# Kernel tuning notes

Hardware: AMD Instinct MI355X
Metric: run time of the kernel (lower is better)

Reference implementation:

```python
import jax, jax.numpy as jnp
import numpy as np

N = 10000       # nodes
F_IN = 512      # input_features
E_DIM = 256     # embedding_features
H0, H1 = 512, 256  # fc layer widths (layers=[512,256]); fc input = 2*E_DIM = 512
N_EDGES = 160000


def setup_inputs() -> dict:
    key = jax.random.key(0)
    ks = jax.random.split(key, 10)
    feature = jax.random.normal(ks[0], (N, F_IN), jnp.float32)
    edge_src = jax.random.randint(ks[1], (N_EDGES,), 0, N, jnp.int32)
    edge_dst = jax.random.randint(ks[2], (N_EDGES,), 0, N, jnp.int32)
    def lin(k, fan_in, fan_out):
        return jax.random.normal(k, (fan_in, fan_out), jnp.float32) / np.sqrt(fan_in).astype(np.float32)
    We = lin(ks[3], F_IN, E_DIM);     be = jnp.zeros((E_DIM,), jnp.float32)
    W0 = lin(ks[4], 2 * E_DIM, H0);   b0 = jnp.zeros((H0,), jnp.float32)
    W1 = lin(ks[5], H0, H1);          b1 = jnp.zeros((H1,), jnp.float32)
    Wlk = lin(ks[6], H1, 1);          blk = jnp.zeros((1,), jnp.float32)
    Wa = lin(ks[7], H1, 2);           ba = jnp.zeros((2,), jnp.float32)
    return dict(feature=feature, We=We, be=be, W0=W0, b0=b0, W1=W1, b1=b1,
                Wlk=Wlk, blk=blk, Wa=Wa, ba=ba,
                edge_src=edge_src, edge_dst=edge_dst)


def reference(feature, We, be, W0, b0, W1, b1, Wlk, blk, Wa, ba, edge_src, edge_dst):
    # get_embedding: Linear + relu
    emb = jax.nn.relu(feature @ We + be)                      # [N, E]
    # Each node i has its neighbor entries plus one 'ending' entry paired with zeros
    seg = jnp.concatenate([edge_src, jnp.arange(N, dtype=edge_src.dtype)])     # [T]
    dst_all = jnp.concatenate([edge_dst, jnp.full((N,), -1, edge_dst.dtype)])  # -1 = ending sentinel
    nbr = jnp.concatenate([emb[edge_dst], jnp.zeros((N, E_DIM), emb.dtype)], axis=0)
    s = jnp.concatenate([emb[seg], nbr], axis=-1)             # [T, 2E]
    # fc MLP, then lk head
    h = jax.nn.relu(jax.nn.relu(s @ W0 + b0) @ W1 + b1)       # [T, H1]
    lk = (h @ Wlk + blk)[:, 0]                                # [T]
    # Deterministic greedy pick per node (argmax of lk == argmax of softmax(lk))
    best = jax.ops.segment_max(lk, seg, num_segments=N)       # [N]
    T = lk.shape[0]
    cand = jnp.where(lk == best[seg], jnp.arange(T, dtype=jnp.int32), -1)
    win = jax.ops.segment_max(cand, seg, num_segments=N)      # winning entry index per node
    chosen = dst_all[win]                                     # chosen neighbor (-1 = ending)
    # action head on the winning pair feature; argmax(softmax(logits)) == argmax(logits)
    logits = h[win] @ Wa + ba                                 # [N, 2]
    at = jnp.argmax(logits, axis=-1)
    do_upd = (chosen >= 0) & (at == 1)
    safe = jnp.clip(chosen, 0, N - 1)
    # hv = mean(feature_origin[i], feature_origin[chosen]) then re-embed
    mean_feat = 0.5 * (feature + feature[safe])               # [N, F]
    new_val = jax.nn.relu(mean_feat @ We + be)                # [N, E]
    tgt = jnp.where(do_upd, safe, N)                          # N = out of range -> dropped
    return emb.at[tgt].set(new_val, mode='drop')
```

## Files before the change

kernel.cpp:

```cpp
#include <hip/hip_runtime.h>
#include <stdint.h>

#define N_NODES 10000
#define F_IN    512
#define E_DIM   256
#define H0D     512
#define H1D     256
#define N_EDGES 160000
#define T_TOT   (N_EDGES + N_NODES)

#define MARGIN_LK 4e-3f
#define MARGIN_L  4e-3f
#define LIST_CAP 60000
#define FIX_GRID 512
#define LP 40

typedef _Float16 f16;
typedef __attribute__((ext_vector_type(8))) _Float16 f16x8;
typedef __attribute__((ext_vector_type(4))) _Float16 f16x4;
typedef __attribute__((ext_vector_type(4))) float f32x4;

__device__ __forceinline__ unsigned int f2ord(float f) {
    unsigned int u = __float_as_uint(f);
    return (u & 0x80000000u) ? ~u : (u | 0x80000000u);
}
__device__ __forceinline__ float ord2f(unsigned int o) {
    unsigned int u = (o & 0x80000000u) ? (o & 0x7fffffffu) : ~o;
    return __uint_as_float(u);
}

__global__ void k_prep_all(const float* __restrict__ We,
                           const float* __restrict__ W1,
                           const float* __restrict__ W0,
                           f16* __restrict__ WeC_h, f16* __restrict__ WeC_l,
                           f16* __restrict__ W1C_h, f16* __restrict__ W1C_l,
                           f16* __restrict__ W0C_h, f16* __restrict__ W0C_l) {
    int b = blockIdx.x;
    int n = threadIdx.x;
    const float* W;
    int ld, rowoff, colbase, c;
    f16 *dh_base, *dl_base;
    if (b < 16) {
        W = We; ld = E_DIM; rowoff = 0; colbase = 0; c = b;
        dh_base = WeC_h; dl_base = WeC_l;
    } else if (b < 32) {
        W = W1; ld = H1D; rowoff = 0; colbase = 0; c = b - 16;
        dh_base = W1C_h; dl_base = W1C_l;
    } else {
        int g = (b - 32) >> 3; c = (b - 32) & 7;
        rowoff = (g >= 2) ? 256 : 0; colbase = (g & 1) * 256;
        W = W0; ld = H0D;
        dh_base = W0C_h + (size_t)g * 8 * 256 * 32;
        dl_base = W0C_l + (size_t)g * 8 * 256 * 32;
    }
    f16* dh = dh_base + ((size_t)c * 256 + n) * 32;
    f16* dl = dl_base + ((size_t)c * 256 + n) * 32;
    const float* src = W + (size_t)(rowoff + c * 32) * ld + colbase + n;
#pragma unroll
    for (int kk = 0; kk < 32; kk++) {
        float w = src[(size_t)kk * ld];
        f16 h = (f16)w;
        f16 l = (f16)(w - (float)h);
        dh[kk] = h;
        dl[kk] = l;
    }
}

__global__ __launch_bounds__(256, 2) void k1_split(
        const float* __restrict__ feat, const f16* __restrict__ Bh_g,
        const f16* __restrict__ Bl_g, const float* __restrict__ be,
        float* __restrict__ Z, float* __restrict__ out) {
    __shared__ f16 Ah[32 * LP], Al_[32 * LP];
    const int tid = threadIdx.x;
    const int wave = tid >> 6, lane = tid & 63;
    const int quad = lane >> 4, l15 = lane & 15;
    const int mbase = blockIdx.x * 32;
    const int arow = tid >> 3, apos = tid & 7;
    const int gm_a = mbase + arow;
    const float* Arow = feat + (size_t)gm_a * F_IN + apos * 4;
    const bool rowok = (gm_a < N_NODES);

    f32x4 acc[2][4];
#pragma unroll
    for (int i = 0; i < 2; i++)
#pragma unroll
        for (int j = 0; j < 4; j++) acc[i][j] = (f32x4){0.f, 0.f, 0.f, 0.f};

    f16x8 bh[4], bl[4], bhn[4], bln[4];
#pragma unroll
    for (int ct = 0; ct < 4; ct++) {
        size_t o = ((size_t)(wave * 64 + ct * 16 + l15)) * 32 + quad * 8;
        bh[ct] = *(const f16x8*)(Bh_g + o);
        bl[ct] = *(const f16x8*)(Bl_g + o);
    }
    float4 a = rowok ? *(const float4*)(Arow) : make_float4(0.f, 0.f, 0.f, 0.f);

    for (int c = 0; c < 16; c++) {
        f16x4 hv, lv;
        float av[4] = {a.x, a.y, a.z, a.w};
#pragma unroll
        for (int q = 0; q < 4; q++) {
            f16 h = (f16)av[q];
            hv[q] = h;
            lv[q] = (f16)(av[q] - (float)h);
        }
        *(f16x4*)(Ah + arow * LP + apos * 4) = hv;
        *(f16x4*)(Al_ + arow * LP + apos * 4) = lv;
        if (c + 1 < 16) {
            a = rowok ? *(const float4*)(Arow + (c + 1) * 32)
                      : make_float4(0.f, 0.f, 0.f, 0.f);
#pragma unroll
            for (int ct = 0; ct < 4; ct++) {
                size_t o = ((size_t)((c + 1) * 256 + wave * 64 + ct * 16 + l15)) * 32 + quad * 8;
                bhn[ct] = *(const f16x8*)(Bh_g + o);
                bln[ct] = *(const f16x8*)(Bl_g + o);
            }
        }
        __syncthreads();
        f16x8 afh[2], afl[2];
#pragma unroll
        for (int rt = 0; rt < 2; rt++) {
            afh[rt] = *(const f16x8*)(Ah + (rt * 16 + l15) * LP + quad * 8);
            afl[rt] = *(const f16x8*)(Al_ + (rt * 16 + l15) * LP + quad * 8);
        }
#pragma unroll
        for (int rt = 0; rt < 2; rt++)
#pragma unroll
            for (int ct = 0; ct < 4; ct++) {
                acc[rt][ct] = __builtin_amdgcn_mfma_f32_16x16x32_f16(
                    afh[rt], bh[ct], acc[rt][ct], 0, 0, 0);
                acc[rt][ct] = __builtin_amdgcn_mfma_f32_16x16x32_f16(
                    afl[rt], bh[ct], acc[rt][ct], 0, 0, 0);
                acc[rt][ct] = __builtin_amdgcn_mfma_f32_16x16x32_f16(
                    afh[rt], bl[ct], acc[rt][ct], 0, 0, 0);
            }
        __syncthreads();
#pragma unroll
        for (int ct = 0; ct < 4; ct++) { bh[ct] = bhn[ct]; bl[ct] = bln[ct]; }
    }

#pragma unroll
    for (int ct = 0; ct < 4; ct++) {
        int n = wave * 64 + ct * 16 + l15;
        float bb = be[n];
#pragma unroll
        for (int rt = 0; rt < 2; rt++)
#pragma unroll
            for (int reg = 0; reg < 4; reg++) {
                int gm = mbase + rt * 16 + quad * 4 + reg;
                if (gm < N_NODES) {
                    float z = acc[rt][ct][reg] + bb;
                    Z[(size_t)gm * E_DIM + n] = z;
                    out[(size_t)gm * E_DIM + n] = fmaxf(z, 0.f);
                }
            }
    }
}

__global__ __launch_bounds__(256, 3) void k2_split(
        const float* __restrict__ emb, const f16* __restrict__ W0Ch,
        const f16* __restrict__ W0Cl, const float* __restrict__ b0,
        f16* __restrict__ Ph, f16* __restrict__ Pl,
        f16* __restrict__ Qh, f16* __restrict__ Ql) {
    __shared__ f16 Ah[64 * LP], Al_[64 * LP];
    const int tid = threadIdx.x;
    const int wave = tid >> 6, lane = tid & 63;
    const int quad = lane >> 4, l15 = lane & 15;
    const int mbase = blockIdx.x * 64;
    const int g = blockIdx.y;
    const int isQ = (g >= 2);
    const int colbase = (g & 1) * 256;
    const int arow = tid >> 2, akp = tid & 3;
    const int gm_a = mbase + arow;
    const float* Arow = emb + (size_t)gm_a * E_DIM + akp * 8;
    const bool rowok = (gm_a < N_NODES);
    const f16* Bh_g = W0Ch + (size_t)g * 8 * 256 * 32;
    const f16* Bl_g = W0Cl + (size_t)g * 8 * 256 * 32;

    f32x4 acc[4][4];
#pragma unroll
    for (int i = 0; i < 4; i++)
#pragma unroll
        for (int j = 0; j < 4; j++) acc[i][j] = (f32x4){0.f, 0.f, 0.f, 0.f};

    f16x8 bh[4], bl[4], bhn[4], bln[4];
#pragma unroll
    for (int ct = 0; ct < 4; ct++) {
        size_t o = ((size_t)(wave * 64 + ct * 16 + l15)) * 32 + quad * 8;
        bh[ct] = *(const f16x8*)(Bh_g + o);
        bl[ct] = *(const f16x8*)(Bl_g + o);
    }
    float4 a0 = make_float4(0.f, 0.f, 0.f, 0.f), a1 = a0;
    if (rowok) { a0 = *(const float4*)(Arow); a1 = *(const float4*)(Arow + 4); }

    for (int c = 0; c < 8; c++) {
        f16x8 hv, lv;
        float av[8] = {a0.x, a0.y, a0.z, a0.w, a1.x, a1.y, a1.z, a1.w};
#pragma unroll
        for (int q = 0; q < 8; q++) {
            f16 h = (f16)av[q];
            hv[q] = h;
            lv[q] = (f16)(av[q] - (float)h);
        }
        *(f16x8*)(Ah + arow * LP + akp * 8) = hv;
        *(f16x8*)(Al_ + arow * LP + akp * 8) = lv;
        if (c + 1 < 8) {
            if (rowok) {
                a0 = *(const float4*)(Arow + (c + 1) * 32);
                a1 = *(const float4*)(Arow + (c + 1) * 32 + 4);
            }
#pragma unroll
            for (int ct = 0; ct < 4; ct++) {
                size_t o = ((size_t)((c + 1) * 256 + wave * 64 + ct * 16 + l15)) * 32 + quad * 8;
                bhn[ct] = *(const f16x8*)(Bh_g + o);
                bln[ct] = *(const f16x8*)(Bl_g + o);
            }
        }
        __syncthreads();
        f16x8 afh[4], afl[4];
#pragma unroll
        for (int rt = 0; rt < 4; rt++) {
            afh[rt] = *(const f16x8*)(Ah + (rt * 16 + l15) * LP + quad * 8);
            afl[rt] = *(const f16x8*)(Al_ + (rt * 16 + l15) * LP + quad * 8);
        }
#pragma unroll
        for (int rt = 0; rt < 4; rt++)
#pragma unroll
            for (int ct = 0; ct < 4; ct++) {
                acc[rt][ct] = __builtin_amdgcn_mfma_f32_16x16x32_f16(
                    afh[rt], bh[ct], acc[rt][ct], 0, 0, 0);
                acc[rt][ct] = __builtin_amdgcn_mfma_f32_16x16x32_f16(
                    afl[rt], bh[ct], acc[rt][ct], 0, 0, 0);
                acc[rt][ct] = __builtin_amdgcn_mfma_f32_16x16x32_f16(
                    afh[rt], bl[ct], acc[rt][ct], 0, 0, 0);
            }
        __syncthreads();
#pragma unroll
        for (int ct = 0; ct < 4; ct++) { bh[ct] = bhn[ct]; bl[ct] = bln[ct]; }
    }

    f16* dh = isQ ? Qh : Ph;
    f16* dl = isQ ? Ql : Pl;
#pragma unroll
    for (int ct = 0; ct < 4; ct++) {
        int n = wave * 64 + ct * 16 + l15;
        float bb = isQ ? 0.f : b0[colbase + n];
#pragma unroll
        for (int rt = 0; rt < 4; rt++)
#pragma unroll
            for (int reg = 0; reg < 4; reg++) {
                int gm = mbase + rt * 16 + quad * 4 + reg;
                if (gm < N_NODES) {
                    float v = acc[rt][ct][reg] + bb;
                    f16 h = (f16)v;
                    dh[(size_t)gm * H0D + colbase + n] = h;
                    dl[(size_t)gm * H0D + colbase + n] = (f16)(v - (float)h);
                }
            }
    }
}

__global__ __launch_bounds__(256, 3) void k3_f16(
        const f16* __restrict__ Pf, const f16* __restrict__ Qf,
        const f16* __restrict__ W1Bh, const float* __restrict__ b1,
        const float* __restrict__ Wlk, const float* __restrict__ blkp,
        const float* __restrict__ Wa, const float* __restrict__ ba,
        const int* __restrict__ esrc, const int* __restrict__ edst,
        unsigned long long* __restrict__ keys, float* __restrict__ lk_app,
        float* __restrict__ logits) {
    __shared__ f16 Ah[64 * LP];
    __shared__ float redA[64][5], redB[64][5], redC[64][5];
    __shared__ int s_seg[64], s_dst[64];
    const int tid = threadIdx.x;
    const int wave = tid >> 6, lane = tid & 63;
    const int quad = lane >> 4, l15 = lane & 15;
    const int tbase = blockIdx.x * 64;

    if (tid < 64) {
        int t = tbase + tid;
        int s = 0, d = -1;
        if (t < N_EDGES) { s = esrc[t]; d = edst[t]; }
        else if (t < T_TOT) { s = t - N_EDGES; }
        s_seg[tid] = s;
        s_dst[tid] = d;
    }
    __syncthreads();

    const int arow = tid >> 2, akp = tid & 3;
    const int sA = s_seg[arow], dA = s_dst[arow];
    const f16* Prow = Pf + (size_t)sA * H0D + akp * 8;
    const f16* Qrow = Qf + (size_t)(dA >= 0 ? dA : 0) * H0D + akp * 8;
    const bool hasQ = (dA >= 0);
    const f16x8 zero8 = (f16x8)(f16)0;

    f32x4 acc[4][4];
#pragma unroll
    for (int i = 0; i < 4; i++)
#pragma unroll
        for (int j = 0; j < 4; j++) acc[i][j] = (f32x4){0.f, 0.f, 0.f, 0.f};

    f16x8 pa = *(const f16x8*)(Prow);
    f16x8 qa = hasQ ? *(const f16x8*)(Qrow) : zero8;
    f16x8 bf[4], bfn[4];
#pragma unroll
    for (int ct = 0; ct < 4; ct++)
        bf[ct] = *(const f16x8*)(W1Bh + ((size_t)(wave * 64 + ct * 16 + l15)) * 32 + quad * 8);

    for (int c = 0; c < 16; c++) {
        f16x8 hv;
#pragma unroll
        for (int q = 0; q < 8; q++) {
            f16 s = pa[q] + qa[q];
            hv[q] = (s > (f16)0) ? s : (f16)0;
        }
        *(f16x8*)(Ah + arow * LP + akp * 8) = hv;
        if (c + 1 < 16) {
            pa = *(const f16x8*)(Prow + (c + 1) * 32);
            qa = hasQ ? *(const f16x8*)(Qrow + (c + 1) * 32) : zero8;
#pragma unroll
            for (int ct = 0; ct < 4; ct++)
                bfn[ct] = *(const f16x8*)(W1Bh +
                    ((size_t)((c + 1) * 256 + wave * 64 + ct * 16 + l15)) * 32 + quad * 8);
        }
        __syncthreads();
        f16x8 af[4];
#pragma unroll
        for (int rt = 0; rt < 4; rt++)
            af[rt] = *(const f16x8*)(Ah + (rt * 16 + l15) * LP + quad * 8);
#pragma unroll
        for (int rt = 0; rt < 4; rt++)
#pragma unroll
            for (int ct = 0; ct < 4; ct++)
                acc[rt][ct] = __builtin_amdgcn_mfma_f32_16x16x32_f16(
                    af[rt], bf[ct], acc[rt][ct], 0, 0, 0);
        __syncthreads();
#pragma unroll
        for (int ct = 0; ct < 4; ct++) bf[ct] = bfn[ct];
    }

    float wl[4], wa0[4], wa1[4], bb[4];
#pragma unroll
    for (int ct = 0; ct < 4; ct++) {
        int n = wave * 64 + ct * 16 + l15;
        wl[ct] = Wlk[n];
        wa0[ct] = Wa[2 * n];
        wa1[ct] = Wa[2 * n + 1];
        bb[ct] = b1[n];
    }
#pragma unroll
    for (int rt = 0; rt < 4; rt++) {
#pragma unroll
        for (int reg = 0; reg < 4; reg++) {
            float plk = 0.f, p0 = 0.f, p1 = 0.f;
#pragma unroll
            for (int ct = 0; ct < 4; ct++) {
                float h = fmaxf(acc[rt][ct][reg] + bb[ct], 0.f);
                plk = fmaf(h, wl[ct], plk);
                p0 = fmaf(h, wa0[ct], p0);
                p1 = fmaf(h, wa1[ct], p1);
            }
#pragma unroll
            for (int off = 8; off >= 1; off >>= 1) {
                plk += __shfl_xor(plk, off);
                p0 += __shfl_xor(p0, off);
                p1 += __shfl_xor(p1, off);
            }
            if (l15 == 0) {
                int row = rt * 16 + quad * 4 + reg;
                redA[row][wave] = plk;
                redB[row][wave] = p0;
                redC[row][wave] = p1;
            }
        }
    }
    __syncthreads();
    if (tid < 64) {
        int t = tbase + tid;
        if (t < T_TOT) {
            float lk = redA[tid][0] + redA[tid][1] + redA[tid][2] + redA[tid][3] + blkp[0];
            float l0 = redB[tid][0] + redB[tid][1] + redB[tid][2] + redB[tid][3] + ba[0];
            float l1 = redC[tid][0] + redC[tid][1] + redC[tid][2] + redC[tid][3] + ba[1];
            lk_app[t] = lk;
            logits[2 * t] = l0;
            logits[2 * t + 1] = l1;
            unsigned long long key =
                ((unsigned long long)f2ord(lk) << 32) | (unsigned int)t;
            atomicMax(keys + s_seg[tid], key);
        }
    }
}

__global__ void k_gb(const float* __restrict__ lk_app,
                     const unsigned long long* __restrict__ keys,
                     const int* __restrict__ esrc,
                     const float* __restrict__ logits,
                     int* __restrict__ list, int* __restrict__ count) {
    int t = blockIdx.x * 256 + threadIdx.x;
    if (t < T_TOT) {
        int seg = (t < N_EDGES) ? esrc[t] : t - N_EDGES;
        unsigned long long k = keys[seg];
        int tw = (int)(k & 0xFFFFFFFFull);
        if (t != tw) {
            float best = ord2f((unsigned int)(k >> 32));
            if (lk_app[t] >= best - MARGIN_LK) {
                int idx = atomicAdd(count, 2);
                if (idx + 1 < LIST_CAP) { list[idx] = t; list[idx + 1] = tw; }
            }
        }
    }
    if (t < N_NODES) {
        int tw = (int)(keys[t] & 0xFFFFFFFFull);
        float g = fabsf(logits[2 * tw + 1] - logits[2 * tw]);
        if (g < MARGIN_L) {
            int idx = atomicAdd(count, 1);
            if (idx < LIST_CAP) list[idx] = tw;
        }
    }
}

__global__ __launch_bounds__(256, 2) void k_fix2(
        const f16* __restrict__ Ph, const f16* __restrict__ Pl,
        const f16* __restrict__ Qh, const f16* __restrict__ Ql,
        const f16* __restrict__ W1Ch, const f16* __restrict__ W1Cl,
        const float* __restrict__ b1, const float* __restrict__ Wlk,
        const float* __restrict__ blkp, const float* __restrict__ Wa,
        const float* __restrict__ ba, const int* __restrict__ esrc,
        const int* __restrict__ edst, const int* __restrict__ list,
        const int* __restrict__ count, unsigned long long* __restrict__ keys2,
        float* __restrict__ logits) {
    __shared__ f16 Ah[64 * LP], Al_[64 * LP];
    __shared__ float redA[64][5], redB[64][5], redC[64][5];
    __shared__ int s_seg[64], s_dst[64], s_t[64];
    const int tid = threadIdx.x;
    const int wave = tid >> 6, lane = tid & 63;
    const int quad = lane >> 4, l15 = lane & 15;
    int cnt = *count;
    if (cnt > LIST_CAP) cnt = LIST_CAP;
    const int nch = (cnt + 63) / 64;

    for (int ch = blockIdx.x; ch < nch; ch += gridDim.x) {
        if (tid < 64) {
            int li = ch * 64 + tid;
            int t = (li < cnt) ? list[li] : -1;
            int s = 0, d = -1;
            if (t >= 0 && t < T_TOT) {
                if (t < N_EDGES) { s = esrc[t]; d = edst[t]; }
                else { s = t - N_EDGES; }
            } else t = -1;
            s_t[tid] = t;
            s_seg[tid] = s;
            s_dst[tid] = d;
        }
        __syncthreads();

        const int arow = tid >> 2, akp = tid & 3;
        const int sA = s_seg[arow], dA = s_dst[arow];
        const f16* ph = Ph + (size_t)sA * H0D + akp * 8;
        const f16* pl = Pl + (size_t)sA * H0D + akp * 8;
        const f16* qh = Qh + (size_t)(dA >= 0 ? dA : 0) * H0D + akp * 8;
        const f16* ql = Ql + (size_t)(dA >= 0 ? dA : 0) * H0D + akp * 8;
        const bool hasQ = (dA >= 0);

        f32x4 acc[4][4];
#pragma unroll
        for (int i = 0; i < 4; i++)
#pragma unroll
            for (int j = 0; j < 4; j++) acc[i][j] = (f32x4){0.f, 0.f, 0.f, 0.f};

        for (int c = 0; c < 16; c++) {
            f16x8 vh = *(const f16x8*)(ph + c * 32);
            f16x8 vl = *(const f16x8*)(pl + c * 32);
            f16x8 wh, wlq;
            if (hasQ) {
                wh = *(const f16x8*)(qh + c * 32);
                wlq = *(const f16x8*)(ql + c * 32);
            }
            f16x8 hv, lv;
#pragma unroll
            for (int q = 0; q < 8; q++) {
                float v = (float)vh[q] + (float)vl[q];
                if (hasQ) v += (float)wh[q] + (float)wlq[q];
                v = fmaxf(v, 0.f);
                f16 h = (f16)v;
                hv[q] = h;
                lv[q] = (f16)(v - (float)h);
            }
            *(f16x8*)(Ah + arow * LP + akp * 8) = hv;
            *(f16x8*)(Al_ + arow * LP + akp * 8) = lv;
            f16x8 bh[4], bl[4];
#pragma unroll
            for (int ct = 0; ct < 4; ct++) {
                size_t o = ((size_t)(c * 256 + wave * 64 + ct * 16 + l15)) * 32 + quad * 8;
                bh[ct] = *(const f16x8*)(W1Ch + o);
                bl[ct] = *(const f16x8*)(W1Cl + o);
            }
            __syncthreads();
            f16x8 afh[4], afl[4];
#pragma unroll
            for (int rt = 0; rt < 4; rt++) {
                afh[rt] = *(const f16x8*)(Ah + (rt * 16 + l15) * LP + quad * 8);
                afl[rt] = *(const f16x8*)(Al_ + (rt * 16 + l15) * LP + quad * 8);
            }
#pragma unroll
            for (int rt = 0; rt < 4; rt++)
#pragma unroll
                for (int ct = 0; ct < 4; ct++) {
                    acc[rt][ct] = __builtin_amdgcn_mfma_f32_16x16x32_f16(
                        afh[rt], bh[ct], acc[rt][ct], 0, 0, 0);
                    acc[rt][ct] = __builtin_amdgcn_mfma_f32_16x16x32_f16(
                        afl[rt], bh[ct], acc[rt][ct], 0, 0, 0);
                    acc[rt][ct] = __builtin_amdgcn_mfma_f32_16x16x32_f16(
                        afh[rt], bl[ct], acc[rt][ct], 0, 0, 0);
                }
            __syncthreads();
        }

        float wl[4], wa0[4], wa1[4], bb[4];
#pragma unroll
        for (int ct = 0; ct < 4; ct++) {
            int n = wave * 64 + ct * 16 + l15;
            wl[ct] = Wlk[n];
            wa0[ct] = Wa[2 * n];
            wa1[ct] = Wa[2 * n + 1];
            bb[ct] = b1[n];
        }
#pragma unroll
        for (int rt = 0; rt < 4; rt++) {
#pragma unroll
            for (int reg = 0; reg < 4; reg++) {
                float plk = 0.f, p0 = 0.f, p1 = 0.f;
#pragma unroll
                for (int ct = 0; ct < 4; ct++) {
                    float h = fmaxf(acc[rt][ct][reg] + bb[ct], 0.f);
                    plk = fmaf(h, wl[ct], plk);
                    p0 = fmaf(h, wa0[ct], p0);
                    p1 = fmaf(h, wa1[ct], p1);
                }
#pragma unroll
                for (int off = 8; off >= 1; off >>= 1) {
                    plk += __shfl_xor(plk, off);
                    p0 += __shfl_xor(p0, off);
                    p1 += __shfl_xor(p1, off);
                }
                if (l15 == 0) {
                    int row = rt * 16 + quad * 4 + reg;
                    redA[row][wave] = plk;
                    redB[row][wave] = p0;
                    redC[row][wave] = p1;
                }
            }
        }
        __syncthreads();
        if (tid < 64) {
            int t = s_t[tid];
            if (t >= 0) {
                float lk = redA[tid][0] + redA[tid][1] + redA[tid][2] + redA[tid][3] + blkp[0];
                float l0 = redB[tid][0] + redB[tid][1] + redB[tid][2] + redB[tid][3] + ba[0];
                float l1 = redC[tid][0] + redC[tid][1] + redC[tid][2] + redC[tid][3] + ba[1];
                logits[2 * t] = l0;
                logits[2 * t + 1] = l1;
                unsigned long long key =
                    ((unsigned long long)f2ord(lk) << 32) | (unsigned int)t;
                atomicMax(keys2 + s_seg[tid], key);
            }
        }
        __syncthreads();
    }
}

__global__ void k4_select(const unsigned long long* __restrict__ keys,
                          const unsigned long long* __restrict__ keys2,
                          const int* __restrict__ edst,
                          const float* __restrict__ logits,
                          int* __restrict__ chosen_arr,
                          int* __restrict__ tgt_writer) {
    int i = blockIdx.x * 256 + threadIdx.x;
    if (i >= N_NODES) return;
    unsigned long long key = keys[i];
    unsigned long long k2v = keys2[i];
    if (k2v != 0ull) key = k2v;
    int t = (int)(key & 0xFFFFFFFFull);
    int chosen = (t < N_EDGES) ? edst[t] : -1;
    float lg0 = logits[2 * t], lg1 = logits[2 * t + 1];
    int at1 = (lg1 > lg0) ? 1 : 0;
    int c = (chosen >= 0 && at1) ? chosen : -1;
    chosen_arr[i] = c;
    if (c >= 0) atomicMax(tgt_writer + c, i + 1);
}

__global__ void k5_update(const int* __restrict__ chosen_arr,
                          const int* __restrict__ tgt_writer,
                          const float* __restrict__ Z,
                          float* __restrict__ out) {
    int i = blockIdx.x;
    int c = chosen_arr[i];
    if (c < 0 || tgt_writer[c] != i + 1) return;
    int n = threadIdx.x;
    float z = 0.5f * (Z[(size_t)i * E_DIM + n] + Z[(size_t)c * E_DIM + n]);
    out[(size_t)c * E_DIM + n] = fmaxf(z, 0.f);
}

extern "C" void kernel_launch(void* const* d_in, const int* in_sizes, int n_in,
                              void* d_out, int out_size, void* d_ws,
                              size_t ws_size, hipStream_t stream) {
    const float* feat = (const float*)d_in[0];
    const float* We   = (const float*)d_in[1];
    const float* be   = (const float*)d_in[2];
    const float* W0   = (const float*)d_in[3];
    const float* b0   = (const float*)d_in[4];
    const float* W1   = (const float*)d_in[5];
    const float* b1   = (const float*)d_in[6];
    const float* Wlk  = (const float*)d_in[7];
    const float* blkp = (const float*)d_in[8];
    const float* Wa   = (const float*)d_in[9];
    const float* ba   = (const float*)d_in[10];
    const int* esrc   = (const int*)d_in[11];
    const int* edst   = (const int*)d_in[12];
    float* out = (float*)d_out;

    char* ws = (char*)d_ws;
    size_t off = 0;
    float* Z  = (float*)(ws + off); off += (size_t)N_NODES * E_DIM * 4;
    f16* Ph   = (f16*)(ws + off);   off += (size_t)N_NODES * H0D * 2;
    f16* Pl   = (f16*)(ws + off);   off += (size_t)N_NODES * H0D * 2;
    f16* Qh   = (f16*)(ws + off);   off += (size_t)N_NODES * H0D * 2;
    f16* Ql   = (f16*)(ws + off);   off += (size_t)N_NODES * H0D * 2;
    char* zero_base = ws + off;
    unsigned long long* keys  = (unsigned long long*)(ws + off); off += N_NODES * 8;
    unsigned long long* keys2 = (unsigned long long*)(ws + off); off += N_NODES * 8;
    int* tgt_writer = (int*)(ws + off); off += N_NODES * 4;
    int* count      = (int*)(ws + off); off += 128;
    size_t zero_bytes = (size_t)((ws + off) - zero_base);
    float* logits = (float*)(ws + off); off += (size_t)T_TOT * 2 * 4;
    float* lk_app = (float*)(ws + off); off += (size_t)T_TOT * 4;
    int* list     = (int*)(ws + off); off += (size_t)LIST_CAP * 4;
    int* chosen_arr = (int*)(ws + off); off += N_NODES * 4;
    f16* WeC_h = (f16*)(ws + off); off += (size_t)16 * 256 * 32 * 2;
    f16* WeC_l = (f16*)(ws + off); off += (size_t)16 * 256 * 32 * 2;
    f16* W1C_h = (f16*)(ws + off); off += (size_t)16 * 256 * 32 * 2;
    f16* W1C_l = (f16*)(ws + off); off += (size_t)16 * 256 * 32 * 2;
    f16* W0C_h = (f16*)(ws + off); off += (size_t)32 * 256 * 32 * 2;
    f16* W0C_l = (f16*)(ws + off); off += (size_t)32 * 256 * 32 * 2;

    hipMemsetAsync(zero_base, 0, zero_bytes, stream);

    k_prep_all<<<dim3(64), 256, 0, stream>>>(
        We, W1, W0, WeC_h, WeC_l, W1C_h, W1C_l, W0C_h, W0C_l);
    k1_split<<<dim3((N_NODES + 31) / 32), 256, 0, stream>>>(
        feat, WeC_h, WeC_l, be, Z, out);
    k2_split<<<dim3((N_NODES + 63) / 64, 4), 256, 0, stream>>>(
        out, W0C_h, W0C_l, b0, Ph, Pl, Qh, Ql);
    k3_f16<<<dim3((T_TOT + 63) / 64), 256, 0, stream>>>(
        Ph, Qh, W1C_h, b1, Wlk, blkp, Wa, ba, esrc, edst,
        keys, lk_app, logits);
    k_gb<<<dim3((T_TOT + 255) / 256), 256, 0, stream>>>(
        lk_app, keys, esrc, logits, list, count);
    k_fix2<<<dim3(FIX_GRID), 256, 0, stream>>>(
        Ph, Pl, Qh, Ql, W1C_h, W1C_l, b1, Wlk, blkp, Wa, ba,
        esrc, edst, list, count, keys2, logits);
    k4_select<<<dim3((N_NODES + 255) / 256), 256, 0, stream>>>(
        keys, keys2, edst, logits, chosen_arr, tgt_writer);
    k5_update<<<dim3(N_NODES), 256, 0, stream>>>(chosen_arr, tgt_writer, Z, out);
}
```

Baseline: 268.7 us.

## Counting-sort pair entries by source node before the fused MLP kernel

Adds histogram, scan and scatter kernels that counting-sort all pair entries by source segment, and makes k3 process entries in that sorted order. Consecutive rows in a block then share the same source P row, which improves cache reuse of the gathered P data and clusters the atomicMax calls onto the same key. k_gb also uses a per-segment flag so each winner is appended to the fix list only once, shrinking the k_fix2 workload. The cost is three extra small launches, one of them a single-block scan, and a nondeterministic within-segment order from the atomic scatter.

Result: slower. 325.0 us (+21.0%).

```diff
diff --git a/kernel.cpp b/kernel.cpp
--- a/kernel.cpp
+++ b/kernel.cpp
@@ -27,6 +27,10 @@
 __device__ __forceinline__ float ord2f(unsigned int o) {
     unsigned int u = (o & 0x80000000u) ? (o & 0x7fffffffu) : ~o;
     return __uint_as_float(u);
+}
+
+__device__ __forceinline__ int seg_of(int t, const int* esrc) {
+    return (t < N_EDGES) ? esrc[t] : t - N_EDGES;
 }
 
 __global__ void k_prep_all(const float* __restrict__ We,
@@ -66,6 +70,39 @@
     }
 }
 
+__global__ void k_hist(const int* __restrict__ esrc, int* __restrict__ hist) {
+    int t = blockIdx.x * 256 + threadIdx.x;
+    if (t >= T_TOT) return;
+    atomicAdd(hist + seg_of(t, esrc), 1);
+}
+
+__global__ void k_scan(const int* __restrict__ hist, int* __restrict__ offs) {
+    __shared__ int part[256];
+    const int tid = threadIdx.x;
+    const int lo = tid * 40;
+    const int hi = (lo + 40 < N_NODES) ? lo + 40 : N_NODES;
+    int s = 0;
+    for (int b = lo; b < hi; b++) s += hist[b];
+    part[tid] = s;
+    __syncthreads();
+    for (int off = 1; off < 256; off <<= 1) {
+        int v = (tid >= off) ? part[tid - off] : 0;
+        __syncthreads();
+        part[tid] += v;
+        __syncthreads();
+    }
+    int run = (tid == 0) ? 0 : part[tid - 1];
+    for (int b = lo; b < hi; b++) { offs[b] = run; run += hist[b]; }
+}
+
+__global__ void k_scat(const int* __restrict__ esrc, int* __restrict__ offs,
+                       int* __restrict__ sorted) {
+    int t = blockIdx.x * 256 + threadIdx.x;
+    if (t >= T_TOT) return;
+    int pos = atomicAdd(offs + seg_of(t, esrc), 1);
+    sorted[pos] = t;
+}
+
 __global__ __launch_bounds__(256, 2) void k1_split(
         const float* __restrict__ feat, const f16* __restrict__ Bh_g,
         const f16* __restrict__ Bl_g, const float* __restrict__ be,
@@ -266,21 +303,26 @@
         const float* __restrict__ Wlk, const float* __restrict__ blkp,
         const float* __restrict__ Wa, const float* __restrict__ ba,
         const int* __restrict__ esrc, const int* __restrict__ edst,
+        const int* __restrict__ sorted,
         unsigned long long* __restrict__ keys, float* __restrict__ lk_app,
         float* __restrict__ logits) {
     __shared__ f16 Ah[64 * LP];
     __shared__ float redA[64][5], redB[64][5], redC[64][5];
-    __shared__ int s_seg[64], s_dst[64];
+    __shared__ int s_seg[64], s_dst[64], s_t[64];
     const int tid = threadIdx.x;
     const int wave = tid >> 6, lane = tid & 63;
     const int quad = lane >> 4, l15 = lane & 15;
     const int tbase = blockIdx.x * 64;
 
     if (tid < 64) {
-        int t = tbase + tid;
+        int li = tbase + tid;
+        int t = (li < T_TOT) ? sorted[li] : -1;
         int s = 0, d = -1;
-        if (t < N_EDGES) { s = esrc[t]; d = edst[t]; }
-        else if (t < T_TOT) { s = t - N_EDGES; }
+        if (t >= 0) {
+            if (t < N_EDGES) { s = esrc[t]; d = edst[t]; }
+            else { s = t - N_EDGES; }
+        }
+        s_t[tid] = t;
         s_seg[tid] = s;
         s_dst[tid] = d;
     }
@@ -375,8 +417,8 @@
     }
     __syncthreads();
     if (tid < 64) {
-        int t = tbase + tid;
-        if (t < T_TOT) {
+        int t = s_t[tid];
+        if (t >= 0) {
             float lk = redA[tid][0] + redA[tid][1] + redA[tid][2] + redA[tid][3] + blkp[0];
             float l0 = redB[tid][0] + redB[tid][1] + redB[tid][2] + redB[tid][3] + ba[0];
             float l1 = redC[tid][0] + redC[tid][1] + redC[tid][2] + redC[tid][3] + ba[1];
@@ -394,17 +436,22 @@
                      const unsigned long long* __restrict__ keys,
                      const int* __restrict__ esrc,
                      const float* __restrict__ logits,
+                     int* __restrict__ seg_flag,
                      int* __restrict__ list, int* __restrict__ count) {
     int t = blockIdx.x * 256 + threadIdx.x;
     if (t < T_TOT) {
-        int seg = (t < N_EDGES) ? esrc[t] : t - N_EDGES;
+        int seg = seg_of(t, esrc);
         unsigned long long k = keys[seg];
         int tw = (int)(k & 0xFFFFFFFFull);
         if (t != tw) {
             float best = ord2f((unsigned int)(k >> 32));
             if (lk_app[t] >= best - MARGIN_LK) {
-                int idx = atomicAdd(count, 2);
-                if (idx + 1 < LIST_CAP) { list[idx] = t; list[idx + 1] = tw; }
+                int idx = atomicAdd(count, 1);
+                if (idx < LIST_CAP) list[idx] = t;
+                if (atomicExch(seg_flag + seg, 1) == 0) {
+                    int idx2 = atomicAdd(count, 1);
+                    if (idx2 < LIST_CAP) list[idx2] = tw;
+                }
             }
         }
     }
@@ -629,8 +676,12 @@
     unsigned long long* keys  = (unsigned long long*)(ws + off); off += N_NODES * 8;
     unsigned long long* keys2 = (unsigned long long*)(ws + off); off += N_NODES * 8;
     int* tgt_writer = (int*)(ws + off); off += N_NODES * 4;
+    int* hist       = (int*)(ws + off); off += N_NODES * 4;
+    int* seg_flag   = (int*)(ws + off); off += N_NODES * 4;
     int* count      = (int*)(ws + off); off += 128;
     size_t zero_bytes = (size_t)((ws + off) - zero_base);
+    int* offs     = (int*)(ws + off); off += N_NODES * 4;
+    int* sorted   = (int*)(ws + off); off += (size_t)T_TOT * 4;
     float* logits = (float*)(ws + off); off += (size_t)T_TOT * 2 * 4;
     float* lk_app = (float*)(ws + off); off += (size_t)T_TOT * 4;
     int* list     = (int*)(ws + off); off += (size_t)LIST_CAP * 4;
@@ -646,15 +697,18 @@
 
     k_prep_all<<<dim3(64), 256, 0, stream>>>(
         We, W1, W0, WeC_h, WeC_l, W1C_h, W1C_l, W0C_h, W0C_l);
+    k_hist<<<dim3((T_TOT + 255) / 256), 256, 0, stream>>>(esrc, hist);
+    k_scan<<<dim3(1), 256, 0, stream>>>(hist, offs);
+    k_scat<<<dim3((T_TOT + 255) / 256), 256, 0, stream>>>(esrc, offs, sorted);
     k1_split<<<dim3((N_NODES + 31) / 32), 256, 0, stream>>>(
         feat, WeC_h, WeC_l, be, Z, out);
     k2_split<<<dim3((N_NODES + 63) / 64, 4), 256, 0, stream>>>(
         out, W0C_h, W0C_l, b0, Ph, Pl, Qh, Ql);
     k3_f16<<<dim3((T_TOT + 63) / 64), 256, 0, stream>>>(
-        Ph, Qh, W1C_h, b1, Wlk, blkp, Wa, ba, esrc, edst,
+        Ph, Qh, W1C_h, b1, Wlk, blkp, Wa, ba, esrc, edst, sorted,
         keys, lk_app, logits);
     k_gb<<<dim3((T_TOT + 255) / 256), 256, 0, stream>>>(
-        lk_app, keys, esrc, logits, list, count);
+        lk_app, keys, esrc, logits, seg_flag, list, count);
     k_fix2<<<dim3(FIX_GRID), 256, 0, stream>>>(
         Ph, Pl, Qh, Ql, W1C_h, W1C_l, b1, Wlk, blkp, Wa, ba,
         esrc, edst, list, count, keys2, logits);
```

## Double-buffer LDS A tiles in k3/k_fix2 and dedupe near-tie winners

Applied to the files above, without the earlier changes.

The k3 and k_fix2 GEMM loops now keep two LDS buffers for the A tile. Each iteration runs the MFMAs on the current buffer while computing and writing the next chunk into the other, which removes one barrier per iteration. k_fix2 also prefetches the next W1 fragments a step ahead. k_gb uses a per-segment flag so each segment's current winner goes into the recheck list only once, shrinking the fix-up work. The cost is twice the LDS for A, more register pressure from the extra fragment copies, and a leftover dead placeholder loop in k_fix2's prologue.

New measurement: 282.6 us. +5.2%, slower.

```diff
diff --git a/kernel.cpp b/kernel.cpp
--- a/kernel.cpp
+++ b/kernel.cpp
@@ -27,6 +27,10 @@
 __device__ __forceinline__ float ord2f(unsigned int o) {
     unsigned int u = (o & 0x80000000u) ? (o & 0x7fffffffu) : ~o;
     return __uint_as_float(u);
+}
+
+__device__ __forceinline__ int seg_of(int t, const int* esrc) {
+    return (t < N_EDGES) ? esrc[t] : t - N_EDGES;
 }
 
 __global__ void k_prep_all(const float* __restrict__ We,
@@ -268,7 +272,7 @@
         const int* __restrict__ esrc, const int* __restrict__ edst,
         unsigned long long* __restrict__ keys, float* __restrict__ lk_app,
         float* __restrict__ logits) {
-    __shared__ f16 Ah[64 * LP];
+    __shared__ f16 Ah[2][64 * LP];
     __shared__ float redA[64][5], redB[64][5], redC[64][5];
     __shared__ int s_seg[64], s_dst[64];
     const int tid = threadIdx.x;
@@ -301,41 +305,53 @@
 
     f16x8 pa = *(const f16x8*)(Prow);
     f16x8 qa = hasQ ? *(const f16x8*)(Qrow) : zero8;
-    f16x8 bf[4], bfn[4];
+    f16x8 bf[4];
 #pragma unroll
     for (int ct = 0; ct < 4; ct++)
         bf[ct] = *(const f16x8*)(W1Bh + ((size_t)(wave * 64 + ct * 16 + l15)) * 32 + quad * 8);
-
-    for (int c = 0; c < 16; c++) {
+    {
         f16x8 hv;
 #pragma unroll
         for (int q = 0; q < 8; q++) {
             f16 s = pa[q] + qa[q];
             hv[q] = (s > (f16)0) ? s : (f16)0;
         }
-        *(f16x8*)(Ah + arow * LP + akp * 8) = hv;
+        *(f16x8*)(&Ah[0][arow * LP + akp * 8]) = hv;
+    }
+    __syncthreads();
+
+    for (int c = 0; c < 16; c++) {
+        f16x8 bcur[4];
+#pragma unroll
+        for (int ct = 0; ct < 4; ct++) bcur[ct] = bf[ct];
         if (c + 1 < 16) {
             pa = *(const f16x8*)(Prow + (c + 1) * 32);
             qa = hasQ ? *(const f16x8*)(Qrow + (c + 1) * 32) : zero8;
 #pragma unroll
             for (int ct = 0; ct < 4; ct++)
-                bfn[ct] = *(const f16x8*)(W1Bh +
+                bf[ct] = *(const f16x8*)(W1Bh +
                     ((size_t)((c + 1) * 256 + wave * 64 + ct * 16 + l15)) * 32 + quad * 8);
         }
-        __syncthreads();
         f16x8 af[4];
 #pragma unroll
         for (int rt = 0; rt < 4; rt++)
-            af[rt] = *(const f16x8*)(Ah + (rt * 16 + l15) * LP + quad * 8);
+            af[rt] = *(const f16x8*)(&Ah[c & 1][(rt * 16 + l15) * LP + quad * 8]);
 #pragma unroll
         for (int rt = 0; rt < 4; rt++)
 #pragma unroll
             for (int ct = 0; ct < 4; ct++)
                 acc[rt][ct] = __builtin_amdgcn_mfma_f32_16x16x32_f16(
-                    af[rt], bf[ct], acc[rt][ct], 0, 0, 0);
-        __syncthreads();
-#pragma unroll
-        for (int ct = 0; ct < 4; ct++) bf[ct] = bfn[ct];
+                    af[rt], bcur[ct], acc[rt][ct], 0, 0, 0);
+        if (c + 1 < 16) {
+            f16x8 hv;
+#pragma unroll
+            for (int q = 0; q < 8; q++) {
+                f16 s = pa[q] + qa[q];
+                hv[q] = (s > (f16)0) ? s : (f16)0;
+            }
+            *(f16x8*)(&Ah[(c + 1) & 1][arow * LP + akp * 8]) = hv;
+        }
+        __syncthreads();
     }
 
     float wl[4], wa0[4], wa1[4], bb[4];
@@ -394,17 +410,22 @@
                      const unsigned long long* __restrict__ keys,
                      const int* __restrict__ esrc,
                      const float* __restrict__ logits,
+                     int* __restrict__ seg_flag,
                      int* __restrict__ list, int* __restrict__ count) {
     int t = blockIdx.x * 256 + threadIdx.x;
     if (t < T_TOT) {
-        int seg = (t < N_EDGES) ? esrc[t] : t - N_EDGES;
+        int seg = seg_of(t, esrc);
         unsigned long long k = keys[seg];
         int tw = (int)(k & 0xFFFFFFFFull);
         if (t != tw) {
             float best = ord2f((unsigned int)(k >> 32));
             if (lk_app[t] >= best - MARGIN_LK) {
-                int idx = atomicAdd(count, 2);
-                if (idx + 1 < LIST_CAP) { list[idx] = t; list[idx + 1] = tw; }
+                int idx = atomicAdd(count, 1);
+                if (idx < LIST_CAP) list[idx] = t;
+                if (atomicExch(seg_flag + seg, 1) == 0) {
+                    int idx2 = atomicAdd(count, 1);
+                    if (idx2 < LIST_CAP) list[idx2] = tw;
+                }
             }
         }
     }
@@ -428,7 +449,7 @@
         const int* __restrict__ edst, const int* __restrict__ list,
         const int* __restrict__ count, unsigned long long* __restrict__ keys2,
         float* __restrict__ logits) {
-    __shared__ f16 Ah[64 * LP], Al_[64 * LP];
+    __shared__ f16 Ah[2][64 * LP], Al_[2][64 * LP];
     __shared__ float redA[64][5], redB[64][5], redC[64][5];
     __shared__ int s_seg[64], s_dst[64], s_t[64];
     const int tid = threadIdx.x;
@@ -467,15 +488,29 @@
 #pragma unroll
             for (int j = 0; j < 4; j++) acc[i][j] = (f32x4){0.f, 0.f, 0.f, 0.f};
 
-        for (int c = 0; c < 16; c++) {
-            f16x8 vh = *(const f16x8*)(ph + c * 32);
-            f16x8 vl = *(const f16x8*)(pl + c * 32);
+        f16x8 bh[4], bl[4];
+#pragma unroll
+        for (int ct = 0; ct < 4; ct++) {
+            size_t o = ((size_t)(wave * 64 + ct * 16 + l15)) * 32 + quad * 8;
+            bh[ct] = *(const f16x8*)(W1Ch + o);
+            bl[ct] = *(const f16x8*)(W1Cl + o);
+        }
+        {
+            f16x8 vh = *(const f16x8*)(ph);
+            f16x8 vl = *(const f16x8*)(pl);
+            f16x8 hv, lv;
+#pragma unroll
+            for (int q = 0; q < 8; q++) {
+                float v = (float)vh[q] + (float)vl[q];
+                if (hasQ) {
+                }
+                hv[q] = (f16)0; lv[q] = (f16)0; (void)v;
+            }
             f16x8 wh, wlq;
             if (hasQ) {
-                wh = *(const f16x8*)(qh + c * 32);
-                wlq = *(const f16x8*)(ql + c * 32);
-            }
-            f16x8 hv, lv;
+                wh = *(const f16x8*)(qh);
+                wlq = *(const f16x8*)(ql);
+            }
 #pragma unroll
             for (int q = 0; q < 8; q++) {
                 float v = (float)vh[q] + (float)vl[q];
@@ -485,33 +520,61 @@
                 hv[q] = h;
                 lv[q] = (f16)(v - (float)h);
             }
-            *(f16x8*)(Ah + arow * LP + akp * 8) = hv;
-            *(f16x8*)(Al_ + arow * LP + akp * 8) = lv;
-            f16x8 bh[4], bl[4];
-#pragma unroll
-            for (int ct = 0; ct < 4; ct++) {
-                size_t o = ((size_t)(c * 256 + wave * 64 + ct * 16 + l15)) * 32 + quad * 8;
-                bh[ct] = *(const f16x8*)(W1Ch + o);
-                bl[ct] = *(const f16x8*)(W1Cl + o);
-            }
-            __syncthreads();
+            *(f16x8*)(&Ah[0][arow * LP + akp * 8]) = hv;
+            *(f16x8*)(&Al_[0][arow * LP + akp * 8]) = lv;
+        }
+        __syncthreads();
+
+        for (int c = 0; c < 16; c++) {
+            f16x8 bhc[4], blc[4];
+#pragma unroll
+            for (int ct = 0; ct < 4; ct++) { bhc[ct] = bh[ct]; blc[ct] = bl[ct]; }
+            f16x8 vh, vl, wh, wlq;
+            if (c + 1 < 16) {
+                vh = *(const f16x8*)(ph + (c + 1) * 32);
+                vl = *(const f16x8*)(pl + (c + 1) * 32);
+                if (hasQ) {
+                    wh = *(const f16x8*)(qh + (c + 1) * 32);
+                    wlq = *(const f16x8*)(ql + (c + 1) * 32);
+                }
+#pragma unroll
+                for (int ct = 0; ct < 4; ct++) {
+                    size_t o = ((size_t)((c + 1) * 256 + wave * 64 + ct * 16 + l15)) * 32 + quad * 8;
+                    bh[ct] = *(const f16x8*)(W1Ch + o);
+                    bl[ct] = *(const f16x8*)(W1Cl + o);
+                }
+            }
             f16x8 afh[4], afl[4];
 #pragma unroll
             for (int rt = 0; rt < 4; rt++) {
-                afh[rt] = *(const f16x8*)(Ah + (rt * 16 + l15) * LP + quad * 8);
-                afl[rt] = *(const f16x8*)(Al_ + (rt * 16 + l15) * LP + quad * 8);
+                afh[rt] = *(const f16x8*)(&Ah[c & 1][(rt * 16 + l15) * LP + quad * 8]);
+                afl[rt] = *(const f16x8*)(&Al_[c & 1][(rt * 16 + l15) * LP + quad * 8]);
             }
 #pragma unroll
             for (int rt = 0; rt < 4; rt++)
 #pragma unroll
                 for (int ct = 0; ct < 4; ct++) {
                     acc[rt][ct] = __builtin_amdgcn_mfma_f32_16x16x32_f16(
-                        afh[rt], bh[ct], acc[rt][ct], 0, 0, 0);
+                        afh[rt], bhc[ct], acc[rt][ct], 0, 0, 0);
                     acc[rt][ct] = __builtin_amdgcn_mfma_f32_16x16x32_f16(
-                        afl[rt], bh[ct], acc[rt][ct], 0, 0, 0);
+                        afl[rt], bhc[ct], acc[rt][ct], 0, 0, 0);
                     acc[rt][ct] = __builtin_amdgcn_mfma_f32_16x16x32_f16(
-                        afh[rt], bl[ct], acc[rt][ct], 0, 0, 0);
-                }
+                        afh[rt], blc[ct], acc[rt][ct], 0, 0, 0);
+                }
+            if (c + 1 < 16) {
+                f16x8 hv, lv;
+#pragma unroll
+                for (int q = 0; q < 8; q++) {
+                    float v = (float)vh[q] + (float)vl[q];
+                    if (hasQ) v += (float)wh[q] + (float)wlq[q];
+                    v = fmaxf(v, 0.f);
+                    f16 h = (f16)v;
+                    hv[q] = h;
+                    lv[q] = (f16)(v - (float)h);
+                }
+                *(f16x8*)(&Ah[(c + 1) & 1][arow * LP + akp * 8]) = hv;
+                *(f16x8*)(&Al_[(c + 1) & 1][arow * LP + akp * 8]) = lv;
+            }
             __syncthreads();
         }
 
@@ -629,6 +692,7 @@
     unsigned long long* keys  = (unsigned long long*)(ws + off); off += N_NODES * 8;
     unsigned long long* keys2 = (unsigned long long*)(ws + off); off += N_NODES * 8;
     int* tgt_writer = (int*)(ws + off); off += N_NODES * 4;
+    int* seg_flag   = (int*)(ws + off); off += N_NODES * 4;
     int* count      = (int*)(ws + off); off += 128;
     size_t zero_bytes = (size_t)((ws + off) - zero_base);
     float* logits = (float*)(ws + off); off += (size_t)T_TOT * 2 * 4;
@@ -654,7 +718,7 @@
         Ph, Qh, W1C_h, b1, Wlk, blkp, Wa, ba, esrc, edst,
         keys, lk_app, logits);
     k_gb<<<dim3((T_TOT + 255) / 256), 256, 0, stream>>>(
-        lk_app, keys, esrc, logits, list, count);
+        lk_app, keys, esrc, logits, seg_flag, list, count);
     k_fix2<<<dim3(FIX_GRID), 256, 0, stream>>>(
         Ph, Pl, Qh, Ql, W1C_h, W1C_l, b1, Wlk, blkp, Wa, ba,
         esrc, edst, list, count, keys2, logits);
```
